# Kernel optimization log

Measured on AMD Instinct MI355X. Metric: run time of the kernel, lower is better.

The kernel has to match this reference:

```python
import jax, jax.numpy as jnp
import numpy as np

B, L, H, N_OUT = 16, 2048, 256, 12
CODEBOOK_VALUE = 1.0


def setup_inputs() -> dict:
    key = jax.random.key(0)
    ks = jax.random.split(key, 7)
    s = 1.0 / np.sqrt(H)  # PyTorch default U(-1/sqrt(H), 1/sqrt(H)) init
    return {
        "embedding": jax.random.normal(ks[0], (B, L, H), jnp.float32),
        # nn.GRU(1, H): weight_ih_l0 is [3H, 1] -> store as vector [3H]
        "w_ih": jax.random.uniform(ks[1], (3 * H,), jnp.float32, -s, s),
        "w_hh": jax.random.uniform(ks[2], (3 * H, H), jnp.float32, -s, s),
        "b_ih": jax.random.uniform(ks[3], (3 * H,), jnp.float32, -s, s),
        "b_hh": jax.random.uniform(ks[4], (3 * H,), jnp.float32, -s, s),
        # nn.Linear(H, 1)
        "w_out": jax.random.uniform(ks[5], (H,), jnp.float32, -s, s),
        "b_out": jax.random.uniform(ks[6], (1,), jnp.float32, -s, s),
    }


def reference(embedding, w_ih, w_hh, b_ih, b_hh, w_out, b_out):
    Bv, Lv, Hv = embedding.shape
    e = embedding.reshape(Bv * Lv, Hv)  # [BL, H]; every step adds e to hidden

    def step(carry, _):
        h, x = carry                      # h: [BL, H], x: [BL] (quantized feedback)
        h_in = h + e                      # hidden fed to GRU is hidden_state + embedding
        # input dim is 1, so W_ih @ x reduces to outer product x * w_ih
        gi = x[:, None] * w_ih[None, :] + b_ih          # [BL, 3H]
        gh = h_in @ w_hh.T + b_hh                        # [BL, 3H]
        gi_r, gi_z, gi_n = jnp.split(gi, 3, axis=-1)     # PyTorch gate order: r, z, n
        gh_r, gh_z, gh_n = jnp.split(gh, 3, axis=-1)
        r = jax.nn.sigmoid(gi_r + gh_r)
        z = jax.nn.sigmoid(gi_z + gh_z)
        n = jnp.tanh(gi_n + r * gh_n)
        h_new = (1.0 - z) * n + z * h_in                 # GRU cell update
        o = h_new @ w_out + b_out[0]                     # [BL] output_layer
        q = jnp.where(o > 0, CODEBOOK_VALUE, -CODEBOOK_VALUE)
        return (h_new, q), (o, q)

    h0 = jnp.zeros_like(e)
    x0 = jnp.zeros((e.shape[0],), e.dtype)
    _, (outs, qs) = jax.lax.scan(step, (h0, x0), None, length=N_OUT)
    # outs/qs: [N_OUT, BL] -> [B, L, N_OUT]
    outputs = jnp.transpose(outs).reshape(Bv, Lv, N_OUT)
    quantized = jnp.transpose(qs).reshape(Bv, Lv, N_OUT)
    return outputs, quantized
```

## Files before the change

### kernel.cpp

```cpp
#include <hip/hip_runtime.h>
#include <math.h>

namespace {
constexpr int kBL = 16 * 2048;
constexpr int kH = 256;
constexpr int kNOut = 12;
constexpr int kRows = 64;
constexpr int kThreads = 512;
constexpr int kAStride = 264;
constexpr int kWhh = 3 * kH * kH;
}

using short8 = __attribute__((ext_vector_type(8))) short;
using f32x4 = __attribute__((ext_vector_type(4))) float;

__device__ inline void bsplit(float v, short& h, short& l) {
  unsigned u = __float_as_uint(v);
  unsigned rh = u + 0x7FFFu + ((u >> 16) & 1u);
  h = (short)(rh >> 16);
  float hf = __uint_as_float(rh & 0xFFFF0000u);
  float r = v - hf;
  unsigned u2 = __float_as_uint(r);
  unsigned rl = u2 + 0x7FFFu + ((u2 >> 16) & 1u);
  l = (short)(rl >> 16);
}

__global__ void split_whh_kernel(const float* __restrict__ w,
                                 short* __restrict__ hi, short* __restrict__ lo) {
  const int i = (blockIdx.x * 256 + threadIdx.x) * 4;
  const float4 v = *reinterpret_cast<const float4*>(w + i);
  short4 h4, l4;
  bsplit(v.x, h4.x, l4.x);
  bsplit(v.y, h4.y, l4.y);
  bsplit(v.z, h4.z, l4.z);
  bsplit(v.w, h4.w, l4.w);
  *reinterpret_cast<short4*>(hi + i) = h4;
  *reinterpret_cast<short4*>(lo + i) = l4;
}

__global__ __launch_bounds__(kThreads, 2)
void rbq_mfma_kernel(const float* __restrict__ emb,
                     const float* __restrict__ w_ih,
                     const float* __restrict__ b_ih,
                     const float* __restrict__ b_hh,
                     const float* __restrict__ w_out,
                     const float* __restrict__ b_out,
                     const short* __restrict__ Bhi,
                     const short* __restrict__ Blo,
                     float* __restrict__ out) {
  __shared__ short Ah[kRows][kAStride];
  __shared__ short Al[kRows][kAStride];
  __shared__ float osc[kRows][9];
  __shared__ float xq[kRows];

  const int tid = threadIdx.x;
  const int lane = tid & 63;
  const int wv = __builtin_amdgcn_readfirstlane(tid >> 6);
  const int grp = lane >> 4;
  const int c16 = lane & 15;
  const int row0 = blockIdx.x * kRows;

  float wihv[3][2], bihv[3][2], bhhv[3][2], woutv[2];
#pragma unroll
  for (int t = 0; t < 2; ++t) {
    const int j = wv * 32 + t * 16 + c16;
#pragma unroll
    for (int g = 0; g < 3; ++g) {
      wihv[g][t] = w_ih[g * kH + j];
      bihv[g][t] = b_ih[g * kH + j];
      bhhv[g][t] = b_hh[g * kH + j];
    }
    woutv[t] = w_out[j];
  }
  const float bo = b_out[0];

  float h_reg[4][4][2];
#pragma unroll
  for (int m = 0; m < 4; ++m)
#pragma unroll
    for (int r = 0; r < 4; ++r)
#pragma unroll
      for (int t = 0; t < 2; ++t) {
        const int rl = m * 16 + grp * 4 + r;
        const int j = wv * 32 + t * 16 + c16;
        const float e = emb[(size_t)(row0 + rl) * kH + j];
        h_reg[m][r][t] = e;
        short hh, hl;
        bsplit(e, hh, hl);
        Ah[rl][j] = hh;
        Al[rl][j] = hl;
      }
  if (tid < kRows) xq[tid] = 0.0f;
  __syncthreads();

  const size_t q_off = (size_t)kBL * kNOut;

  for (int step = 0; step < kNOut; ++step) {
    f32x4 acc[4][2][3];
#pragma unroll
    for (int m = 0; m < 4; ++m)
#pragma unroll
      for (int t = 0; t < 2; ++t)
#pragma unroll
        for (int g = 0; g < 3; ++g) {
          const float b = bhhv[g][t];
          acc[m][t][g] = f32x4{b, b, b, b};
        }

#pragma unroll 2
    for (int kc = 0; kc < 8; ++kc) {
      short8 ah[4], al[4];
#pragma unroll
      for (int m = 0; m < 4; ++m) {
        const int rr = m * 16 + c16;
        const int cc = kc * 32 + grp * 8;
        ah[m] = *reinterpret_cast<const short8*>(&Ah[rr][cc]);
        al[m] = *reinterpret_cast<const short8*>(&Al[rr][cc]);
      }
#pragma unroll
      for (int g = 0; g < 3; ++g)
#pragma unroll
        for (int t = 0; t < 2; ++t) {
          const size_t bidx =
              (size_t)(g * kH + wv * 32 + t * 16 + c16) * kH + kc * 32 + grp * 8;
          const short8 bh = *reinterpret_cast<const short8*>(Bhi + bidx);
          const short8 bl = *reinterpret_cast<const short8*>(Blo + bidx);
#pragma unroll
          for (int m = 0; m < 4; ++m) {
            acc[m][t][g] = __builtin_amdgcn_mfma_f32_16x16x32_bf16(ah[m], bh, acc[m][t][g], 0, 0, 0);
            acc[m][t][g] = __builtin_amdgcn_mfma_f32_16x16x32_bf16(al[m], bh, acc[m][t][g], 0, 0, 0);
            acc[m][t][g] = __builtin_amdgcn_mfma_f32_16x16x32_bf16(ah[m], bl, acc[m][t][g], 0, 0, 0);
          }
        }
    }
    __syncthreads();

    float opart[4][4];
#pragma unroll
    for (int m = 0; m < 4; ++m)
#pragma unroll
      for (int r = 0; r < 4; ++r) opart[m][r] = 0.0f;

#pragma unroll
    for (int m = 0; m < 4; ++m) {
#pragma unroll
      for (int r = 0; r < 4; ++r) {
        const int rl = m * 16 + grp * 4 + r;
        const float x = xq[rl];
#pragma unroll
        for (int t = 0; t < 2; ++t) {
          const int j = wv * 32 + t * 16 + c16;
          const float ghr = acc[m][t][0][r];
          const float ghz = acc[m][t][1][r];
          const float ghn = acc[m][t][2][r];
          const float gr = fmaf(x, wihv[0][t], bihv[0][t]) + ghr;
          const float gz = fmaf(x, wihv[1][t], bihv[1][t]) + ghz;
          const float gni = fmaf(x, wihv[2][t], bihv[2][t]);
          const float rg = 1.0f / (1.0f + __expf(-gr));
          const float zg = 1.0f / (1.0f + __expf(-gz));
          const float ta = gni + rg * ghn;
          const float at = fabsf(ta);
          const float et = __expf(-2.0f * at);
          const float th = copysignf((1.0f - et) / (1.0f + et), ta);
          const float hprev = h_reg[m][r][t];
          const float hn = fmaf(zg, hprev - th, th);
          opart[m][r] = fmaf(hn, woutv[t], opart[m][r]);
          const float hnext = hn + emb[(size_t)(row0 + rl) * kH + j];
          h_reg[m][r][t] = hnext;
          short hh, hl;
          bsplit(hnext, hh, hl);
          Ah[rl][j] = hh;
          Al[rl][j] = hl;
        }
      }
    }

#pragma unroll
    for (int m = 0; m < 4; ++m)
#pragma unroll
      for (int r = 0; r < 4; ++r) {
#pragma unroll
        for (int mask = 1; mask < 16; mask <<= 1)
          opart[m][r] += __shfl_xor(opart[m][r], mask, 64);
      }
    float ov = opart[0][0];
#pragma unroll
    for (int mm = 0; mm < 4; ++mm)
#pragma unroll
      for (int rr = 0; rr < 4; ++rr)
        if (c16 == mm * 4 + rr) ov = opart[mm][rr];
    osc[(c16 >> 2) * 16 + grp * 4 + (c16 & 3)][wv] = ov;
    __syncthreads();

    if (tid < kRows) {
      float s = bo;
#pragma unroll
      for (int w2 = 0; w2 < 8; ++w2) s += osc[tid][w2];
      const float q = s > 0.0f ? 1.0f : -1.0f;
      const size_t gr = (size_t)(row0 + tid);
      out[gr * kNOut + step] = s;
      out[q_off + gr * kNOut + step] = q;
      xq[tid] = q;
    }
    __syncthreads();
  }
}

extern "C" void kernel_launch(void* const* d_in, const int* in_sizes, int n_in,
                              void* d_out, int out_size, void* d_ws, size_t ws_size,
                              hipStream_t stream) {
  (void)in_sizes; (void)n_in; (void)out_size; (void)ws_size;
  const float* emb = (const float*)d_in[0];
  const float* w_ih = (const float*)d_in[1];
  const float* w_hh = (const float*)d_in[2];
  const float* b_ih = (const float*)d_in[3];
  const float* b_hh = (const float*)d_in[4];
  const float* w_out = (const float*)d_in[5];
  const float* b_out = (const float*)d_in[6];

  short* Bhi = (short*)d_ws;
  short* Blo = Bhi + kWhh;

  split_whh_kernel<<<kWhh / (256 * 4), 256, 0, stream>>>(w_hh, Bhi, Blo);
  rbq_mfma_kernel<<<kBL / kRows, kThreads, 0, stream>>>(
      emb, w_ih, b_ih, b_hh, w_out, b_out, Bhi, Blo, (float*)d_out);
}
```

Before: 763.8 us.

## Split GRU hidden columns across 16 waves and drop trailing per-step barrier

The block grows from 8 to 16 waves, so each wave owns 16 hidden columns instead of 32. That halves the per-thread accumulators, hidden state and gate constants, cutting register pressure and adding more waves to hide latency. The k-loop is reordered so the three gate B fragments are loaded once per k-chunk and reused across the four row tiles, and the output-projection reduction writes directly from lane 0 of each 16-lane group. The final per-step barrier is removed because the next step's first barrier already orders the xq and osc accesses. In exchange, every wave now reads the full A tile from LDS, which doubles LDS read traffic.

Result: faster. 738.5 us (-3.3%).

```diff
diff --git a/kernel.cpp b/kernel.cpp
--- a/kernel.cpp
+++ b/kernel.cpp
@@ -6,8 +6,8 @@
 constexpr int kH = 256;
 constexpr int kNOut = 12;
 constexpr int kRows = 64;
-constexpr int kThreads = 512;
-constexpr int kAStride = 264;
+constexpr int kThreads = 1024;
+constexpr int kS = 264;
 constexpr int kWhh = 3 * kH * kH;
 }
 
@@ -38,19 +38,21 @@
   *reinterpret_cast<short4*>(lo + i) = l4;
 }
 
-__global__ __launch_bounds__(kThreads, 2)
-void rbq_mfma_kernel(const float* __restrict__ emb,
-                     const float* __restrict__ w_ih,
-                     const float* __restrict__ b_ih,
-                     const float* __restrict__ b_hh,
-                     const float* __restrict__ w_out,
-                     const float* __restrict__ b_out,
-                     const short* __restrict__ Bhi,
-                     const short* __restrict__ Blo,
-                     float* __restrict__ out) {
-  __shared__ short Ah[kRows][kAStride];
-  __shared__ short Al[kRows][kAStride];
-  __shared__ float osc[kRows][9];
+#define MFMA(A, B, C) __builtin_amdgcn_mfma_f32_16x16x32_bf16((A), (B), (C), 0, 0, 0)
+
+__global__ __launch_bounds__(kThreads, 4)
+void rbq_mfma3_kernel(const float* __restrict__ emb,
+                      const float* __restrict__ w_ih,
+                      const float* __restrict__ b_ih,
+                      const float* __restrict__ b_hh,
+                      const float* __restrict__ w_out,
+                      const float* __restrict__ b_out,
+                      const short* __restrict__ Bh,
+                      const short* __restrict__ Bl,
+                      float* __restrict__ out) {
+  __shared__ short Ah[kRows][kS];
+  __shared__ short Al[kRows][kS];
+  __shared__ float osc[kRows][17];
   __shared__ float xq[kRows];
 
   const int tid = threadIdx.x;
@@ -59,119 +61,91 @@
   const int grp = lane >> 4;
   const int c16 = lane & 15;
   const int row0 = blockIdx.x * kRows;
-
-  float wihv[3][2], bihv[3][2], bhhv[3][2], woutv[2];
-#pragma unroll
-  for (int t = 0; t < 2; ++t) {
-    const int j = wv * 32 + t * 16 + c16;
-#pragma unroll
-    for (int g = 0; g < 3; ++g) {
-      wihv[g][t] = w_ih[g * kH + j];
-      bihv[g][t] = b_ih[g * kH + j];
-      bhhv[g][t] = b_hh[g * kH + j];
-    }
-    woutv[t] = w_out[j];
-  }
+  const int j = wv * 16 + c16;
+
+  const float wihr = w_ih[j], wihz = w_ih[kH + j], wihn = w_ih[2 * kH + j];
+  const float bihr = b_ih[j], bihz = b_ih[kH + j], bihn = b_ih[2 * kH + j];
+  const float bhhr = b_hh[j], bhhz = b_hh[kH + j], bhhn = b_hh[2 * kH + j];
+  const float wo = w_out[j];
   const float bo = b_out[0];
-
-  float h_reg[4][4][2];
+  const size_t q_off = (size_t)kBL * kNOut;
+
+  float h_reg[4][4];
 #pragma unroll
   for (int m = 0; m < 4; ++m)
 #pragma unroll
-    for (int r = 0; r < 4; ++r)
-#pragma unroll
-      for (int t = 0; t < 2; ++t) {
-        const int rl = m * 16 + grp * 4 + r;
-        const int j = wv * 32 + t * 16 + c16;
-        const float e = emb[(size_t)(row0 + rl) * kH + j];
-        h_reg[m][r][t] = e;
-        short hh, hl;
-        bsplit(e, hh, hl);
-        Ah[rl][j] = hh;
-        Al[rl][j] = hl;
-      }
+    for (int r = 0; r < 4; ++r) {
+      const int rl = m * 16 + grp * 4 + r;
+      const float e = emb[(size_t)(row0 + rl) * kH + j];
+      h_reg[m][r] = e;
+      short hh, hl;
+      bsplit(e, hh, hl);
+      Ah[rl][j] = hh;
+      Al[rl][j] = hl;
+    }
   if (tid < kRows) xq[tid] = 0.0f;
   __syncthreads();
 
-  const size_t q_off = (size_t)kBL * kNOut;
-
   for (int step = 0; step < kNOut; ++step) {
-    f32x4 acc[4][2][3];
-#pragma unroll
-    for (int m = 0; m < 4; ++m)
-#pragma unroll
-      for (int t = 0; t < 2; ++t)
-#pragma unroll
-        for (int g = 0; g < 3; ++g) {
-          const float b = bhhv[g][t];
-          acc[m][t][g] = f32x4{b, b, b, b};
-        }
-
-#pragma unroll 2
+    f32x4 acc[4][3];
+#pragma unroll
+    for (int m = 0; m < 4; ++m) {
+      acc[m][0] = f32x4{bhhr, bhhr, bhhr, bhhr};
+      acc[m][1] = f32x4{bhhz, bhhz, bhhz, bhhz};
+      acc[m][2] = f32x4{bhhn, bhhn, bhhn, bhhn};
+    }
+
+#pragma unroll 1
     for (int kc = 0; kc < 8; ++kc) {
-      short8 ah[4], al[4];
+      const int ko = kc * 32 + grp * 8;
+      short8 bh[3], bl[3];
+#pragma unroll
+      for (int g = 0; g < 3; ++g) {
+        const size_t base = (size_t)(g * kH + j) * kH + ko;
+        bh[g] = *reinterpret_cast<const short8*>(Bh + base);
+        bl[g] = *reinterpret_cast<const short8*>(Bl + base);
+      }
 #pragma unroll
       for (int m = 0; m < 4; ++m) {
-        const int rr = m * 16 + c16;
-        const int cc = kc * 32 + grp * 8;
-        ah[m] = *reinterpret_cast<const short8*>(&Ah[rr][cc]);
-        al[m] = *reinterpret_cast<const short8*>(&Al[rr][cc]);
-      }
-#pragma unroll
-      for (int g = 0; g < 3; ++g)
-#pragma unroll
-        for (int t = 0; t < 2; ++t) {
-          const size_t bidx =
-              (size_t)(g * kH + wv * 32 + t * 16 + c16) * kH + kc * 32 + grp * 8;
-          const short8 bh = *reinterpret_cast<const short8*>(Bhi + bidx);
-          const short8 bl = *reinterpret_cast<const short8*>(Blo + bidx);
-#pragma unroll
-          for (int m = 0; m < 4; ++m) {
-            acc[m][t][g] = __builtin_amdgcn_mfma_f32_16x16x32_bf16(ah[m], bh, acc[m][t][g], 0, 0, 0);
-            acc[m][t][g] = __builtin_amdgcn_mfma_f32_16x16x32_bf16(al[m], bh, acc[m][t][g], 0, 0, 0);
-            acc[m][t][g] = __builtin_amdgcn_mfma_f32_16x16x32_bf16(ah[m], bl, acc[m][t][g], 0, 0, 0);
-          }
-        }
+        const short8 ah = *reinterpret_cast<const short8*>(&Ah[m * 16 + c16][ko]);
+        const short8 al = *reinterpret_cast<const short8*>(&Al[m * 16 + c16][ko]);
+#pragma unroll
+        for (int g = 0; g < 3; ++g) acc[m][g] = MFMA(ah, bh[g], acc[m][g]);
+#pragma unroll
+        for (int g = 0; g < 3; ++g) acc[m][g] = MFMA(al, bh[g], acc[m][g]);
+#pragma unroll
+        for (int g = 0; g < 3; ++g) acc[m][g] = MFMA(ah, bl[g], acc[m][g]);
+      }
     }
     __syncthreads();
 
     float opart[4][4];
-#pragma unroll
-    for (int m = 0; m < 4; ++m)
-#pragma unroll
-      for (int r = 0; r < 4; ++r) opart[m][r] = 0.0f;
-
 #pragma unroll
     for (int m = 0; m < 4; ++m) {
 #pragma unroll
       for (int r = 0; r < 4; ++r) {
         const int rl = m * 16 + grp * 4 + r;
         const float x = xq[rl];
-#pragma unroll
-        for (int t = 0; t < 2; ++t) {
-          const int j = wv * 32 + t * 16 + c16;
-          const float ghr = acc[m][t][0][r];
-          const float ghz = acc[m][t][1][r];
-          const float ghn = acc[m][t][2][r];
-          const float gr = fmaf(x, wihv[0][t], bihv[0][t]) + ghr;
-          const float gz = fmaf(x, wihv[1][t], bihv[1][t]) + ghz;
-          const float gni = fmaf(x, wihv[2][t], bihv[2][t]);
-          const float rg = 1.0f / (1.0f + __expf(-gr));
-          const float zg = 1.0f / (1.0f + __expf(-gz));
-          const float ta = gni + rg * ghn;
-          const float at = fabsf(ta);
-          const float et = __expf(-2.0f * at);
-          const float th = copysignf((1.0f - et) / (1.0f + et), ta);
-          const float hprev = h_reg[m][r][t];
-          const float hn = fmaf(zg, hprev - th, th);
-          opart[m][r] = fmaf(hn, woutv[t], opart[m][r]);
-          const float hnext = hn + emb[(size_t)(row0 + rl) * kH + j];
-          h_reg[m][r][t] = hnext;
-          short hh, hl;
-          bsplit(hnext, hh, hl);
-          Ah[rl][j] = hh;
-          Al[rl][j] = hl;
-        }
+        const float ghr = acc[m][0][r];
+        const float ghz = acc[m][1][r];
+        const float ghn = acc[m][2][r];
+        const float gr = fmaf(x, wihr, bihr) + ghr;
+        const float gz = fmaf(x, wihz, bihz) + ghz;
+        const float gni = fmaf(x, wihn, bihn);
+        const float rg = 1.0f / (1.0f + __expf(-gr));
+        const float zg = 1.0f / (1.0f + __expf(-gz));
+        const float ta = gni + rg * ghn;
+        const float at = fabsf(ta);
+        const float et = __expf(-2.0f * at);
+        const float th = copysignf((1.0f - et) / (1.0f + et), ta);
+        const float hn = fmaf(zg, h_reg[m][r] - th, th);
+        opart[m][r] = hn * wo;
+        const float hnext = hn + emb[(size_t)(row0 + rl) * kH + j];
+        h_reg[m][r] = hnext;
+        short hh, hl;
+        bsplit(hnext, hh, hl);
+        Ah[rl][j] = hh;
+        Al[rl][j] = hl;
       }
     }
 
@@ -181,28 +155,27 @@
       for (int r = 0; r < 4; ++r) {
 #pragma unroll
         for (int mask = 1; mask < 16; mask <<= 1)
-          opart[m][r] += __shfl_xor(opart[m][r], mask, 64);
-      }
-    float ov = opart[0][0];
-#pragma unroll
-    for (int mm = 0; mm < 4; ++mm)
-#pragma unroll
-      for (int rr = 0; rr < 4; ++rr)
-        if (c16 == mm * 4 + rr) ov = opart[mm][rr];
-    osc[(c16 >> 2) * 16 + grp * 4 + (c16 & 3)][wv] = ov;
+          opart[m][r] += __shfl_xor(opart[m][r], mask, 16);
+      }
+    if (c16 == 0) {
+#pragma unroll
+      for (int m = 0; m < 4; ++m)
+#pragma unroll
+        for (int r = 0; r < 4; ++r)
+          osc[m * 16 + grp * 4 + r][wv] = opart[m][r];
+    }
     __syncthreads();
 
     if (tid < kRows) {
       float s = bo;
 #pragma unroll
-      for (int w2 = 0; w2 < 8; ++w2) s += osc[tid][w2];
+      for (int w2 = 0; w2 < 16; ++w2) s += osc[tid][w2];
       const float q = s > 0.0f ? 1.0f : -1.0f;
       const size_t gr = (size_t)(row0 + tid);
       out[gr * kNOut + step] = s;
       out[q_off + gr * kNOut + step] = q;
       xq[tid] = q;
     }
-    __syncthreads();
   }
 }
 
@@ -218,10 +191,10 @@
   const float* w_out = (const float*)d_in[5];
   const float* b_out = (const float*)d_in[6];
 
-  short* Bhi = (short*)d_ws;
-  short* Blo = Bhi + kWhh;
-
-  split_whh_kernel<<<kWhh / (256 * 4), 256, 0, stream>>>(w_hh, Bhi, Blo);
-  rbq_mfma_kernel<<<kBL / kRows, kThreads, 0, stream>>>(
-      emb, w_ih, b_ih, b_hh, w_out, b_out, Bhi, Blo, (float*)d_out);
-}
+  short* Bh = (short*)d_ws;
+  short* Bl = Bh + kWhh;
+
+  split_whh_kernel<<<kWhh / (256 * 4), 256, 0, stream>>>(w_hh, Bh, Bl);
+  rbq_mfma3_kernel<<<kBL / kRows, kThreads, 0, stream>>>(
+      emb, w_ih, b_ih, b_hh, w_out, b_out, Bh, Bl, (float*)d_out);
+}
```
